# Kernel optimization log

Hardware: AMD Instinct MI355X
Metric: run time of the kernel (lower is better)

## Reference

```python
import jax, jax.numpy as jnp
import numpy as np


def _mlp(x, W0, b0, W1, b1, W2, b2, W3, b3):
    # 4-layer MLP, ReLU between layers, no final activation
    h = jax.nn.relu(x @ W0 + b0)
    h = jax.nn.relu(h @ W1 + b1)
    h = jax.nn.relu(h @ W2 + b2)
    return h @ W3 + b3


def setup_inputs() -> dict:
    key = jax.random.key(0)
    ks = jax.random.split(key, 8)
    B, t, p, f = 4, 12, 32, 64          # num_graphs, timesteps, n_patches, nhid
    n = 10000                            # nodes per graph
    E = 200000                           # subgraph-node membership entries
    in_dim = f * t + t                   # 780
    horizon = 12
    scale = 0.02
    return {
        "mixer_x": jax.random.normal(ks[0], (B, t, p, f), jnp.float32),
        "features": jax.random.normal(ks[1], (B * n, t), jnp.float32),
        "subgraphs_batch": jax.random.randint(ks[2], (E,), 0, p * B),
        "subgraphs_nodes_mapper": jax.random.randint(ks[3], (E,), 0, n * B),
        "W0": jax.random.normal(ks[4], (in_dim, in_dim), jnp.float32) * scale,
        "b0": jnp.zeros((in_dim,), jnp.float32),
        "W1": jax.random.normal(ks[5], (in_dim, in_dim), jnp.float32) * scale,
        "b1": jnp.zeros((in_dim,), jnp.float32),
        "W2": jax.random.normal(ks[6], (in_dim, in_dim), jnp.float32) * scale,
        "b2": jnp.zeros((in_dim,), jnp.float32),
        "W3": jax.random.normal(ks[7], (in_dim, horizon), jnp.float32) * scale,
        "b3": jnp.zeros((horizon,), jnp.float32),
    }


def reference(mixer_x, features, subgraphs_batch, subgraphs_nodes_mapper,
              W0, b0, W1, b1, W2, b2, W3, b3):
    B, t, p, f = mixer_x.shape
    n_seg = features.shape[0]                      # n * B segments
    n = n_seg // B
    # passthrough: '(B n) t -> B n t'
    passthrough = features.reshape(B, n, t)
    # mixer_x: 'B t p f -> (p B) t f'
    flat = jnp.transpose(mixer_x, (2, 0, 1, 3)).reshape(p * B, t, f)
    # gather by subgraph index, then scatter-mean over node mapper
    gathered = flat[subgraphs_batch]               # (E, t, f)
    sums = jax.ops.segment_sum(gathered, subgraphs_nodes_mapper, num_segments=n_seg)
    counts = jax.ops.segment_sum(jnp.ones((gathered.shape[0],), gathered.dtype),
                                 subgraphs_nodes_mapper, num_segments=n_seg)
    nodes = sums / jnp.maximum(counts, 1.0)[:, None, None]   # (n*B, t, f)
    # '(n B) t f -> B n (t f)'
    nodes = jnp.transpose(nodes.reshape(n, B, t, f), (1, 0, 2, 3)).reshape(B, n, t * f)
    mlp_in = jnp.concatenate([passthrough, nodes], axis=-1)  # (B, n, t + t*f)
    mlp_out = _mlp(mlp_in, W0, b0, W1, b1, W2, b2, W3, b3)   # (B, n, horizon)
    # 'B n h -> (B n) h'
    return mlp_out.reshape(B * n, -1)
```

## Files before the change

kernel.cpp:

```cpp
#include <hip/hip_runtime.h>

#define BG    4
#define TT    12
#define NN    10000
#define EN    200000
#define NSEG  40000
#define NROWS 40000
#define MPAD  40064
#define KD    800
#define KA0   160
#define NPW   896
#define NT    7

typedef __attribute__((ext_vector_type(8))) short bf8_t;
typedef __attribute__((ext_vector_type(4))) float f4_t;

__device__ __forceinline__ unsigned short f2bf(float x) {
  unsigned int u = __float_as_uint(x);
  u += 0x7fffu + ((u >> 16) & 1u);
  return (unsigned short)(u >> 16);
}

#define GLDS16(src, dst) __builtin_amdgcn_global_load_lds( \
    (const __attribute__((address_space(1))) void*)(src),  \
    (__attribute__((address_space(3))) void*)(dst), 16, 0, 0)

__global__ void k_zero(int* counts) {
  int i = blockIdx.x * 256 + threadIdx.x;
  if (i < NSEG) counts[i] = 0;
}

__global__ void k_count(const int* __restrict__ mapper, int* __restrict__ counts) {
  int e = blockIdx.x * 256 + threadIdx.x;
  if (e < EN) atomicAdd(&counts[mapper[e]], 1);
}

__global__ void k_zerof(float* __restrict__ p, int n) {
  int i = blockIdx.x * 256 + threadIdx.x;
  if (i < n) p[i] = 0.f;
}

__global__ void k_scatterCf(const int* __restrict__ mapper, const int* __restrict__ batch,
                            float* __restrict__ Cff) {
  int e = blockIdx.x * 256 + threadIdx.x;
  if (e < EN) {
    const int s = mapper[e];
    const int r = (s % BG) * NN + s / BG;
    atomicAdd(&Cff[(size_t)r * 128 + batch[e]], 1.0f);
  }
}

__global__ void k_buildA(const float* __restrict__ features, const int* __restrict__ counts,
                         const float* __restrict__ Cff, unsigned short* __restrict__ A) {
  int idx = blockIdx.x * 256 + threadIdx.x;
  if (idx >= MPAD * KA0) return;
  const int r = idx / KA0, c = idx - r * KA0;
  float v = 0.f;
  if (r < NROWS) {
    if (c < 12) {
      v = features[(size_t)r * TT + c];
    } else if (c < 140) {
      const int s = (r % NN) * BG + (r / NN);
      const int cnt = counts[s];
      const float inv = 1.f / (float)(cnt > 0 ? cnt : 1);
      v = Cff[(size_t)r * 128 + (c - 12)] * inv;
    }
  }
  A[idx] = f2bf(v);
}

__global__ void k_buildB(const float* __restrict__ W0, const float* __restrict__ fW0,
                         unsigned short* __restrict__ WTB) {
  int idx = blockIdx.x * 256 + threadIdx.x;
  if (idx >= NPW * KA0) return;
  const int n = idx / KA0, k = idx - n * KA0;
  float v = 0.f;
  if (n < 780) {
    if (k < 12) v = W0[(size_t)k * 780 + n];
    else if (k < 140) v = fW0[(size_t)(k - 12) * KD + n];
  }
  WTB[idx] = f2bf(v);
}

__global__ void k_tpad(const float* __restrict__ W, unsigned short* __restrict__ Wt,
                       int ldw, int nsrc, int total) {
  int idx = blockIdx.x * 256 + threadIdx.x;
  if (idx >= total) return;
  int n = idx / KD, k = idx % KD;
  float v = (n < nsrc && k < 780) ? W[k * ldw + n] : 0.f;
  Wt[idx] = f2bf(v);
}

__global__ void k_padbias3(const float* __restrict__ b0, const float* __restrict__ b1,
                           const float* __restrict__ b2, float* __restrict__ p0,
                           float* __restrict__ p1, float* __restrict__ p2) {
  int i = blockIdx.x * 256 + threadIdx.x;
  if (i >= 3 * KD) return;
  const int which = i / KD, c = i - which * KD;
  const float* src = which == 0 ? b0 : (which == 1 ? b1 : b2);
  float* dst = which == 0 ? p0 : (which == 1 ? p1 : p2);
  dst[c] = (c < 780) ? src[c] : 0.f;
}

__global__ __launch_bounds__(256) void k_flatW0(const float* __restrict__ mixer,
                                                const float* __restrict__ W0,
                                                float* __restrict__ fW0) {
  __shared__ float sA[8][768];
  __shared__ float sRed[4][64][9];
  const int tid = threadIdx.x;
  const int c0 = blockIdx.x * 64, j0 = blockIdx.y * 8;
  for (int i = tid; i < 8 * 768; i += 256) {
    int jj = i / 768;
    int k = i - jj * 768;
    int j = j0 + jj;
    int tt = k >> 6, ff = k & 63;
    sA[jj][k] = mixer[(((j & 3) * TT + tt) * 32 + (j >> 2)) * 64 + ff];
  }
  __syncthreads();
  const int cc = tid & 63, ks = tid >> 6;
  const int c = c0 + cc;
  float acc[8] = {};
  if (c < 780) {
    const float* wp = W0 + (size_t)(12 + ks * 192) * 780 + c;
    #pragma unroll 4
    for (int k = ks * 192; k < ks * 192 + 192; ++k) {
      const float w = *wp; wp += 780;
      #pragma unroll
      for (int jj = 0; jj < 8; ++jj) acc[jj] = fmaf(sA[jj][k], w, acc[jj]);
    }
  }
  #pragma unroll
  for (int jj = 0; jj < 8; ++jj) sRed[ks][cc][jj] = acc[jj];
  __syncthreads();
  for (int o = tid; o < 512; o += 256) {
    const int oc = o & 63, jj = o >> 6;
    const int wc = c0 + oc;
    if (wc < KD) {
      float s = sRed[0][oc][jj] + sRed[1][oc][jj] + sRed[2][oc][jj] + sRed[3][oc][jj];
      fW0[(size_t)(j0 + jj) * KD + wc] = s;
    }
  }
}

template<int KA>
__global__ __launch_bounds__(256) void gemm_relu(
    const unsigned short* __restrict__ A, const unsigned short* __restrict__ WT,
    const float* __restrict__ bias, unsigned short* __restrict__ C) {
  __shared__ unsigned short sA[128 * 32];
  __shared__ unsigned short sB[128 * 32];
  const int tid = threadIdx.x, lane = tid & 63, wid = tid >> 6;
  const int wm = wid >> 1, wn = wid & 1;

  const int nwg = gridDim.x;
  const int q = nwg >> 3, r8 = nwg & 7;
  const int xcd = blockIdx.x & 7, idx = blockIdx.x >> 3;
  const int linear = (xcd < r8 ? xcd * (q + 1) : r8 * (q + 1) + (xcd - r8) * q) + idx;
  const int rowtile = linear / NT, ntile = linear - rowtile * NT;

  const int row0 = rowtile * 128, n0 = ntile * 128;
  const char* gA = (const char*)A + (size_t)row0 * (KA * 2);
  const char* gB = (const char*)WT + (size_t)n0 * (KA * 2);
  const int frow = lane & 15, fk = (lane >> 4) * 8;

  f4_t acc[4][4] = {};

  for (int kt = 0; kt < KA / 32; ++kt) {
    const int kb = kt * 64;
    __syncthreads();
    #pragma unroll
    for (int L = 0; L < 2; ++L) {
      const int segb = L * 256 + wid * 64;
      const int seg = segb + lane;
      const size_t go = (size_t)(seg >> 2) * (KA * 2) + kb + (seg & 3) * 16;
      GLDS16(gA + go, (char*)sA + segb * 16);
      GLDS16(gB + go, (char*)sB + segb * 16);
    }
    __syncthreads();
    bf8_t af[4], bf[4];
    #pragma unroll
    for (int mi = 0; mi < 4; ++mi)
      af[mi] = *(const bf8_t*)(sA + (wm * 64 + mi * 16 + frow) * 32 + fk);
    #pragma unroll
    for (int ni = 0; ni < 4; ++ni)
      bf[ni] = *(const bf8_t*)(sB + (wn * 64 + ni * 16 + frow) * 32 + fk);
    #pragma unroll
    for (int mi = 0; mi < 4; ++mi)
      #pragma unroll
      for (int ni = 0; ni < 4; ++ni)
        acc[mi][ni] = __builtin_amdgcn_mfma_f32_16x16x32_bf16(bf[ni], af[mi], acc[mi][ni], 0, 0, 0);
  }

  const int cq = (lane >> 4) * 4;
  #pragma unroll
  for (int mi = 0; mi < 4; ++mi) {
    const int r = row0 + wm * 64 + mi * 16 + frow;
    unsigned short* crow = C + (size_t)r * KD;
    #pragma unroll
    for (int ni = 0; ni < 4; ++ni) {
      const int c = n0 + wn * 64 + ni * 16 + cq;
      if (c < KD) {
        f4_t v = acc[mi][ni];
        const f4_t bb = *(const f4_t*)(bias + c);
        float v0 = fmaxf(v[0] + bb[0], 0.f);
        float v1 = fmaxf(v[1] + bb[1], 0.f);
        float v2 = fmaxf(v[2] + bb[2], 0.f);
        float v3 = fmaxf(v[3] + bb[3], 0.f);
        uint2 pk;
        pk.x = (unsigned int)f2bf(v0) | ((unsigned int)f2bf(v1) << 16);
        pk.y = (unsigned int)f2bf(v2) | ((unsigned int)f2bf(v3) << 16);
        *(uint2*)(crow + c) = pk;
      }
    }
  }
}

__global__ __launch_bounds__(256) void gemm_out(
    const unsigned short* __restrict__ A, const unsigned short* __restrict__ WT3,
    const float* __restrict__ b3, float* __restrict__ out) {
  __shared__ unsigned short sA[128 * 32];
  __shared__ unsigned short sB[16 * 32];
  const int tid = threadIdx.x, lane = tid & 63, wid = tid >> 6;
  const int row0 = blockIdx.x * 128;
  const char* gA = (const char*)A + (size_t)row0 * (KD * 2);
  const char* gB = (const char*)WT3;
  const int frow = lane & 15, fk = (lane >> 4) * 8;

  f4_t acc[2] = {};

  for (int kt = 0; kt < 25; ++kt) {
    const int kb = kt * 64;
    __syncthreads();
    #pragma unroll
    for (int L = 0; L < 2; ++L) {
      const int segb = L * 256 + wid * 64;
      const int seg = segb + lane;
      GLDS16(gA + (size_t)(seg >> 2) * (KD * 2) + kb + (seg & 3) * 16, (char*)sA + segb * 16);
    }
    if (wid == 0) {
      const int seg = lane;
      GLDS16(gB + (size_t)(seg >> 2) * (KD * 2) + kb + (seg & 3) * 16, (char*)sB);
    }
    __syncthreads();
    const bf8_t bf = *(const bf8_t*)(sB + frow * 32 + fk);
    #pragma unroll
    for (int mi = 0; mi < 2; ++mi) {
      const bf8_t af = *(const bf8_t*)(sA + (wid * 32 + mi * 16 + frow) * 32 + fk);
      acc[mi] = __builtin_amdgcn_mfma_f32_16x16x32_bf16(bf, af, acc[mi], 0, 0, 0);
    }
  }

  const int cg = (lane >> 4) * 4;
  #pragma unroll
  for (int mi = 0; mi < 2; ++mi) {
    const int r = row0 + wid * 32 + mi * 16 + frow;
    if (r < NROWS && cg < 12) {
      f4_t v = acc[mi];
      const f4_t bb = *(const f4_t*)(b3 + cg);
      v += bb;
      *(f4_t*)(out + (size_t)r * 12 + cg) = v;
    }
  }
}

extern "C" void kernel_launch(void* const* d_in, const int* in_sizes, int n_in,
                              void* d_out, int out_size, void* d_ws, size_t ws_size,
                              hipStream_t stream) {
  const float* mixer    = (const float*)d_in[0];
  const float* features = (const float*)d_in[1];
  const int*   sg_batch = (const int*)d_in[2];
  const int*   sg_map   = (const int*)d_in[3];
  const float* W0 = (const float*)d_in[4];  const float* b0 = (const float*)d_in[5];
  const float* W1 = (const float*)d_in[6];  const float* b1 = (const float*)d_in[7];
  const float* W2 = (const float*)d_in[8];  const float* b2 = (const float*)d_in[9];
  const float* W3 = (const float*)d_in[10]; const float* b3 = (const float*)d_in[11];
  float* out = (float*)d_out;

  char* wsp = (char*)d_ws;
  auto alloc = [&](size_t bytes) { char* p = wsp; wsp += (bytes + 255) & ~(size_t)255; return p; };
  unsigned short* h0  = (unsigned short*)alloc((size_t)MPAD * KD * 2);
  unsigned short* h1  = (unsigned short*)alloc((size_t)MPAD * KD * 2);
  unsigned short* Wt1 = (unsigned short*)alloc((size_t)NPW * KD * 2);
  unsigned short* Wt2 = (unsigned short*)alloc((size_t)NPW * KD * 2);
  unsigned short* Wt3 = (unsigned short*)alloc((size_t)16 * KD * 2);
  unsigned short* WTB = (unsigned short*)alloc((size_t)NPW * KA0 * 2);
  float* bp0   = (float*)alloc(KD * 4);
  float* bp1   = (float*)alloc(KD * 4);
  float* bp2   = (float*)alloc(KD * 4);
  float* fW0   = (float*)alloc((size_t)128 * KD * 4);
  int* counts  = (int*)alloc(NSEG * 4);
  float* Cff = (float*)h1;
  unsigned short* Abuf = (unsigned short*)((char*)h1 + ((size_t)MPAD * 128 * 4 + 255 & ~(size_t)255));

  k_zero<<<(NSEG + 255) / 256, 256, 0, stream>>>(counts);
  k_count<<<(EN + 255) / 256, 256, 0, stream>>>(sg_map, counts);

  k_zerof<<<(MPAD * 128 + 255) / 256, 256, 0, stream>>>(Cff, MPAD * 128);
  k_scatterCf<<<(EN + 255) / 256, 256, 0, stream>>>(sg_map, sg_batch, Cff);

  k_flatW0<<<dim3(13, 16), 256, 0, stream>>>(mixer, W0, fW0);
  k_tpad<<<(NPW * KD + 255) / 256, 256, 0, stream>>>(W1, Wt1, 780, 780, NPW * KD);
  k_tpad<<<(NPW * KD + 255) / 256, 256, 0, stream>>>(W2, Wt2, 780, 780, NPW * KD);
  k_tpad<<<(16 * KD + 255) / 256, 256, 0, stream>>>(W3, Wt3, 12, 12, 16 * KD);
  k_padbias3<<<(3 * KD + 255) / 256, 256, 0, stream>>>(b0, b1, b2, bp0, bp1, bp2);
  k_buildB<<<(NPW * KA0 + 255) / 256, 256, 0, stream>>>(W0, fW0, WTB);

  k_buildA<<<(MPAD * KA0 + 255) / 256, 256, 0, stream>>>(features, counts, Cff, Abuf);

  gemm_relu<KA0><<<(MPAD / 128) * NT, 256, 0, stream>>>(Abuf, WTB, bp0, h0);

  gemm_relu<KD><<<(MPAD / 128) * NT, 256, 0, stream>>>(h0, Wt1, bp1, h1);
  gemm_relu<KD><<<(MPAD / 128) * NT, 256, 0, stream>>>(h1, Wt2, bp2, h0);

  gemm_out<<<MPAD / 128, 256, 0, stream>>>(h0, Wt3, b3, out);
}
```

Measured before the change: 380.0 us.

## Double-buffer LDS tiles in gemm_relu to overlap global loads with MFMA

The GEMM main loop now uses two LDS buffers for the A and B tiles. The next K-tile is fetched with global_load_lds while MFMAs run on the current one, which halves the barriers per iteration and hides global-load latency behind compute. Load address offsets are also hoisted out of the loop. In exchange, LDS use doubles to 32 KB per block, which may reduce occupancy, and correctness relies on the barrier waiting for the async LDS loads.

```diff
diff --git a/kernel.cpp b/kernel.cpp
--- a/kernel.cpp
+++ b/kernel.cpp
@@ -146,15 +146,15 @@
 __global__ __launch_bounds__(256) void gemm_relu(
     const unsigned short* __restrict__ A, const unsigned short* __restrict__ WT,
     const float* __restrict__ bias, unsigned short* __restrict__ C) {
-  __shared__ unsigned short sA[128 * 32];
-  __shared__ unsigned short sB[128 * 32];
+  __shared__ unsigned short sA[2][128 * 32];
+  __shared__ unsigned short sB[2][128 * 32];
   const int tid = threadIdx.x, lane = tid & 63, wid = tid >> 6;
   const int wm = wid >> 1, wn = wid & 1;
 
   const int nwg = gridDim.x;
   const int q = nwg >> 3, r8 = nwg & 7;
-  const int xcd = blockIdx.x & 7, idx = blockIdx.x >> 3;
-  const int linear = (xcd < r8 ? xcd * (q + 1) : r8 * (q + 1) + (xcd - r8) * q) + idx;
+  const int xcd = blockIdx.x & 7, bidx = blockIdx.x >> 3;
+  const int linear = (xcd < r8 ? xcd * (q + 1) : r8 * (q + 1) + (xcd - r8) * q) + bidx;
   const int rowtile = linear / NT, ntile = linear - rowtile * NT;
 
   const int row0 = rowtile * 128, n0 = ntile * 128;
@@ -162,33 +162,49 @@
   const char* gB = (const char*)WT + (size_t)n0 * (KA * 2);
   const int frow = lane & 15, fk = (lane >> 4) * 8;
 
+  const int seg0 = wid * 64 + lane;
+  const int seg1 = 256 + wid * 64 + lane;
+  const size_t roff0 = (size_t)(seg0 >> 2) * (KA * 2) + (seg0 & 3) * 16;
+  const size_t roff1 = (size_t)(seg1 >> 2) * (KA * 2) + (seg1 & 3) * 16;
+  const int loff0 = (wid * 64) * 16;
+  const int loff1 = (256 + wid * 64) * 16;
+
   f4_t acc[4][4] = {};
 
-  for (int kt = 0; kt < KA / 32; ++kt) {
+  auto stage = [&](int buf, int kt) {
     const int kb = kt * 64;
-    __syncthreads();
-    #pragma unroll
-    for (int L = 0; L < 2; ++L) {
-      const int segb = L * 256 + wid * 64;
-      const int seg = segb + lane;
-      const size_t go = (size_t)(seg >> 2) * (KA * 2) + kb + (seg & 3) * 16;
-      GLDS16(gA + go, (char*)sA + segb * 16);
-      GLDS16(gB + go, (char*)sB + segb * 16);
-    }
-    __syncthreads();
-    bf8_t af[4], bf[4];
+    GLDS16(gA + roff0 + kb, (char*)sA[buf] + loff0);
+    GLDS16(gB + roff0 + kb, (char*)sB[buf] + loff0);
+    GLDS16(gA + roff1 + kb, (char*)sA[buf] + loff1);
+    GLDS16(gB + roff1 + kb, (char*)sB[buf] + loff1);
+  };
+
+  auto compute = [&](int buf) {
+    bf8_t af[4], bfr[4];
     #pragma unroll
     for (int mi = 0; mi < 4; ++mi)
-      af[mi] = *(const bf8_t*)(sA + (wm * 64 + mi * 16 + frow) * 32 + fk);
+      af[mi] = *(const bf8_t*)(&sA[buf][(wm * 64 + mi * 16 + frow) * 32 + fk]);
     #pragma unroll
     for (int ni = 0; ni < 4; ++ni)
-      bf[ni] = *(const bf8_t*)(sB + (wn * 64 + ni * 16 + frow) * 32 + fk);
+      bfr[ni] = *(const bf8_t*)(&sB[buf][(wn * 64 + ni * 16 + frow) * 32 + fk]);
     #pragma unroll
     for (int mi = 0; mi < 4; ++mi)
       #pragma unroll
       for (int ni = 0; ni < 4; ++ni)
-        acc[mi][ni] = __builtin_amdgcn_mfma_f32_16x16x32_bf16(bf[ni], af[mi], acc[mi][ni], 0, 0, 0);
-  }
+        acc[mi][ni] = __builtin_amdgcn_mfma_f32_16x16x32_bf16(bfr[ni], af[mi], acc[mi][ni], 0, 0, 0);
+  };
+
+  constexpr int NKT = KA / 32;
+  stage(0, 0);
+  __syncthreads();
+  int cur = 0;
+  for (int kt = 0; kt < NKT - 1; ++kt) {
+    stage(cur ^ 1, kt + 1);
+    compute(cur);
+    __syncthreads();
+    cur ^= 1;
+  }
+  compute(cur);
 
   const int cq = (lane >> 4) * 4;
   #pragma unroll
```

Measured after the change: 424.6 us. +11.7%, slower.
